# Performance work log

Measured on AMD Instinct MI355X. Metric: run time of the kernel, lower is better.

Reference implementation:

```python
import jax, jax.numpy as jnp
import numpy as np

HEAD_NUMS = 8
LN_EPS = 1e-5


def _layernorm(x, g, b):
    m = jnp.mean(x, axis=-1, keepdims=True)
    v = jnp.var(x, axis=-1, keepdims=True)
    return (x - m) * jax.lax.rsqrt(v + LN_EPS) * g + b


def setup_inputs() -> dict:
    key = jax.random.key(0)
    ks = jax.random.split(key, 6)
    B, S, D = 4, 2048, 512
    x = jax.random.normal(ks[0], (B, S, D), dtype=jnp.float32)
    W1 = jax.random.normal(ks[1], (4 * D, D), dtype=jnp.float32) * 0.02
    b1 = jnp.zeros((4 * D,), dtype=jnp.float32)
    ln_g = jnp.ones((D,), dtype=jnp.float32)
    ln_b = jnp.zeros((D,), dtype=jnp.float32)
    W2 = jax.random.normal(ks[2], (D, D), dtype=jnp.float32) * 0.02
    b2 = jnp.zeros((D,), dtype=jnp.float32)
    return {"x": x, "W1": W1, "b1": b1, "ln_g": ln_g, "ln_b": ln_b, "W2": W2, "b2": b2}


def reference(x, W1, b1, ln_g, ln_b, W2, b2):
    B, S, D = x.shape
    H = HEAD_NUMS
    hd = D // H
    # fused qkv+gate projection with SiLU (HSTU style)
    h = jax.nn.silu(x @ W1.T + b1)                   # [B,S,4D]
    h = h.reshape(B, S, 4, H, hd)                    # split into gate,q,k,v
    gate = jnp.transpose(h[:, :, 0], (0, 2, 1, 3))   # [B,H,S,hd]
    q = jnp.transpose(h[:, :, 1], (0, 2, 1, 3))
    k = jnp.transpose(h[:, :, 2], (0, 2, 1, 3))
    v = jnp.transpose(h[:, :, 3], (0, 2, 1, 3))
    scale = 1.0 / np.sqrt(hd).astype(np.float32)
    scores = jnp.einsum('bhsd,bhtd->bhst', q, k) * scale   # [B,H,S,S]
    causal = jnp.tril(jnp.ones((S, S), dtype=bool))        # allowed: t <= s
    # silu replaces softmax; masked (future) positions contribute 0
    # (mathematical limit of silu(-inf) is 0)
    a = jnp.where(causal, jax.nn.silu(scores), 0.0)
    o = jnp.einsum('bhst,bhtd->bhsd', a, v)                # [B,H,S,hd]
    o = jnp.transpose(o, (0, 2, 1, 3)).reshape(B, S, D)
    normed = _layernorm(o, ln_g, ln_b)
    gate_f = jnp.transpose(gate, (0, 2, 1, 3)).reshape(B, S, D)
    return (normed * gate_f) @ W2.T + b2
```

## Files before the change

kernel.cpp:

```cpp
#include <hip/hip_runtime.h>
#include <hip/hip_bf16.h>
#include <cstdint>


typedef __attribute__((ext_vector_type(8))) short short8;
typedef __attribute__((ext_vector_type(4))) float f32x4;

__device__ __forceinline__ unsigned short f2bf(float f) {
  union { float f; unsigned u; } v; v.f = f;
  unsigned r = v.u + 0x7FFFu + ((v.u >> 16) & 1u);
  return (unsigned short)(r >> 16);
}
__device__ __forceinline__ float bf2f(unsigned short h) {
  union { unsigned u; float f; } v; v.u = ((unsigned)h) << 16; return v.f;
}
__device__ __forceinline__ float fast_rcp(float x) {
#if __has_builtin(__builtin_amdgcn_rcpf)
  return __builtin_amdgcn_rcpf(x);
#else
  return 1.0f / x;
#endif
}
__device__ __forceinline__ float fast_exp2(float x) {
#if __has_builtin(__builtin_amdgcn_exp2f)
  return __builtin_amdgcn_exp2f(x);
#else
  return exp2f(x);
#endif
}
__device__ __forceinline__ float silu_f(float x) {
  return x * fast_rcp(1.0f + fast_exp2(-1.442695041f * x));
}
__device__ __forceinline__ unsigned pk2(float lo, float hi) {
  union { __hip_bfloat162 b; unsigned u; } cv;
  cv.b = __float22bfloat162_rn(make_float2(lo, hi));
  return cv.u;
}
__device__ __forceinline__ void gl_lds16(const void* g, void* l) {
  __builtin_amdgcn_global_load_lds(
      (const __attribute__((address_space(1))) void*)g,
      (__attribute__((address_space(3))) void*)l, 16, 0, 0);
}

__global__ void convert_kernel(const float* __restrict__ x, const float* __restrict__ w1,
                               const float* __restrict__ w2,
                               unsigned short* __restrict__ xb, unsigned short* __restrict__ w1b,
                               unsigned short* __restrict__ w2b) {
  int i = blockIdx.x * 256 + threadIdx.x;
  const float* s; unsigned short* d;
  if (i < 1048576) { s = x; d = xb; }
  else if (i < 1048576 + 262144) { i -= 1048576; s = w1; d = w1b; }
  else { i -= (1048576 + 262144); if (i >= 65536) return; s = w2; d = w2b; }
  float4 f = ((const float4*)s)[i];
  uint2 o; o.x = pk2(f.x, f.y); o.y = pk2(f.z, f.w);
  ((uint2*)d)[i] = o;
}

__global__ __launch_bounds__(256, 2) void gemm1_kernel(
    const unsigned short* __restrict__ xb,
    const unsigned short* __restrict__ w1b,
    const float* __restrict__ b1,
    unsigned short* __restrict__ h,
    unsigned short* __restrict__ vt)
{
  __shared__ __align__(16) unsigned short smem[16896];
  unsigned short* As = smem;
  unsigned short* Bs = smem + 8192;
  const int tid = threadIdx.x;
  const int w = tid >> 6, l = tid & 63;
  const int bm = blockIdx.x & 63, bn = blockIdx.x >> 6;
  const int wm = w & 1, wn = w >> 1;
  const int quad = l >> 4, lc = l & 15, lc7 = lc & 7;
  const int r8 = l >> 3, c8 = (l & 7) ^ r8;

  f32x4 acc[4][4] = {};
  const unsigned short* ga = xb + (size_t)(bm * 128 + w * 32 + r8) * 512 + c8 * 8;
  const unsigned short* gb = w1b + (size_t)(bn * 128 + w * 32 + r8) * 512 + c8 * 8;

  for (int kt = 0; kt < 512; kt += 64) {
#pragma unroll
    for (int i = 0; i < 4; ++i) {
      gl_lds16(ga + i * 8 * 512 + kt, As + (w * 4 + i) * 512);
      gl_lds16(gb + i * 8 * 512 + kt, Bs + (w * 4 + i) * 512);
    }
    __syncthreads();
#pragma unroll
    for (int kk = 0; kk < 2; ++kk) {
      short8 af[4], bf[4];
#pragma unroll
      for (int mt = 0; mt < 4; ++mt)
        af[mt] = *(const short8*)(As + (wm * 64 + mt * 16 + lc) * 64 +
                                  (((kk * 4 + quad) ^ lc7) * 8));
#pragma unroll
      for (int nt = 0; nt < 4; ++nt)
        bf[nt] = *(const short8*)(Bs + (wn * 64 + nt * 16 + lc) * 64 +
                                  (((kk * 4 + quad) ^ lc7) * 8));
#pragma unroll
      for (int mt = 0; mt < 4; ++mt)
#pragma unroll
        for (int nt = 0; nt < 4; ++nt)
          acc[mt][nt] = __builtin_amdgcn_mfma_f32_16x16x32_bf16(af[mt], bf[nt], acc[mt][nt], 0, 0, 0);
    }
    __syncthreads();
  }

  unsigned short* T = smem;
  const int sec = bn >> 2;
  if (sec == 3) {
#pragma unroll
    for (int nt = 0; nt < 4; ++nt) {
      const int nl = wn * 64 + nt * 16 + lc;
      const float bias = b1[bn * 128 + nl];
#pragma unroll
      for (int mt = 0; mt < 4; ++mt) {
        const int sl = wm * 64 + mt * 16 + quad * 4;
        uint2 pk;
        pk.x = pk2(silu_f(acc[mt][nt][0] + bias), silu_f(acc[mt][nt][1] + bias));
        pk.y = pk2(silu_f(acc[mt][nt][2] + bias), silu_f(acc[mt][nt][3] + bias));
        *(uint2*)(T + nl * 132 + sl) = pk;
      }
    }
  } else {
    const float osc = (sec == 1) ? 0.125f : 1.0f;
#pragma unroll
    for (int nt = 0; nt < 4; ++nt) {
      const int nl = wn * 64 + nt * 16 + lc;
      const float bias = b1[bn * 128 + nl];
#pragma unroll
      for (int mt = 0; mt < 4; ++mt) {
        const int sl = wm * 64 + mt * 16 + quad * 4;
#pragma unroll
        for (int r = 0; r < 4; ++r)
          T[(sl + r) * 132 + nl] = f2bf(silu_f(acc[mt][nt][r] + bias) * osc);
      }
    }
  }
  __syncthreads();
  const int rrow = tid >> 4, rcol = (tid & 15) * 8;
  if (sec == 3) {
    const int bq = bm >> 4, sbase = (bm & 15) * 128;
#pragma unroll
    for (int p = 0; p < 8; ++p) {
      const int row = p * 16 + rrow;
      const int n = bn * 128 + row, hh = (n >> 6) & 7, d = n & 63;
      *(short8*)(vt + (size_t)((bq * 8 + hh) * 64 + d) * 2048 + sbase + rcol) =
          *(const short8*)(T + row * 132 + rcol);
    }
  } else {
#pragma unroll
    for (int p = 0; p < 8; ++p) {
      const int row = p * 16 + rrow;
      *(short8*)(h + (size_t)(bm * 128 + row) * 2048 + bn * 128 + rcol) =
          *(const short8*)(T + row * 132 + rcol);
    }
  }
}

__global__ __launch_bounds__(256, 3) void attn_kernel(
    const unsigned short* __restrict__ h,
    const unsigned short* __restrict__ vt,
    float* __restrict__ o)
{
  __shared__ __align__(16) unsigned short Ks[128 * 64];
  __shared__ __align__(16) unsigned short Vs[64 * 128];
  __shared__ __align__(16) unsigned short Ps[64 * 136];
  const int tid = threadIdx.x;
  const int w = tid >> 6, l = tid & 63;
  const int bh = blockIdx.x & 31;
  const int qi = 31 - (blockIdx.x >> 5);
  const int b = bh >> 3, hh = bh & 7;
  const int quad = l >> 4, lc = l & 15, lc7 = lc & 7;
  const int r8 = l >> 3, c8 = (l & 7) ^ r8;
  const int wm = w & 1, wn = w >> 1;
  const int q0 = qi * 64;
  const int nk = (qi >> 1) + 1;

  {
    const unsigned short* qg =
        h + (size_t)(b * 2048 + q0 + w * 16 + r8) * 2048 + 512 + hh * 64 + c8 * 8;
#pragma unroll
    for (int i = 0; i < 2; ++i)
      gl_lds16(qg + (size_t)i * 8 * 2048, Ks + (w * 2 + i) * 512);
  }
  __syncthreads();
  short8 qf[2][2];
#pragma unroll
  for (int nt = 0; nt < 2; ++nt)
#pragma unroll
    for (int kk = 0; kk < 2; ++kk)
      qf[nt][kk] = *(const short8*)(Ks + (wn * 32 + nt * 16 + lc) * 64 +
                                    (((kk * 4 + quad) ^ lc7) * 8));

  f32x4 oacc[4] = {};

  const unsigned short* kg =
      h + (size_t)(b * 2048 + w * 32 + r8) * 2048 + 1024 + hh * 64 + c8 * 8;
  const int vrow = l >> 4, vcol = l & 15;
  const unsigned short* vgE =
      vt + (size_t)(bh * 64 + w * 16 + vrow) * 2048 + ((vcol ^ vrow) * 8);
  const unsigned short* vgO =
      vt + (size_t)(bh * 64 + w * 16 + vrow) * 2048 + ((vcol ^ vrow ^ 4) * 8);

  for (int ti = 0; ti < nk; ++ti) {
    __syncthreads();
    const int toff = ti * 128;
#pragma unroll
    for (int i = 0; i < 4; ++i) {
      gl_lds16(kg + (size_t)(toff + i * 8) * 2048, Ks + (w * 4 + i) * 512);
      const unsigned short* vsrc = ((i & 1) ? vgO : vgE) + (size_t)(i * 4) * 2048 + toff;
      gl_lds16(vsrc, Vs + (w * 4 + i) * 512);
    }
    __syncthreads();

    f32x4 sc[4][2] = {};
#pragma unroll
    for (int kk = 0; kk < 2; ++kk) {
      short8 kf[4];
#pragma unroll
      for (int mt = 0; mt < 4; ++mt)
        kf[mt] = *(const short8*)(Ks + (wm * 64 + mt * 16 + lc) * 64 +
                                  (((kk * 4 + quad) ^ lc7) * 8));
#pragma unroll
      for (int mt = 0; mt < 4; ++mt)
#pragma unroll
        for (int nt = 0; nt < 2; ++nt)
          sc[mt][nt] = __builtin_amdgcn_mfma_f32_16x16x32_bf16(kf[mt], qf[nt][kk], sc[mt][nt], 0, 0, 0);
    }

    if (ti < nk - 1) {
#pragma unroll
      for (int mt = 0; mt < 4; ++mt) {
        const int tloc = wm * 64 + mt * 16 + quad * 4;
#pragma unroll
        for (int nt = 0; nt < 2; ++nt) {
          const int qloc = wn * 32 + nt * 16 + lc;
          uint2 pk;
          pk.x = pk2(silu_f(sc[mt][nt][0]), silu_f(sc[mt][nt][1]));
          pk.y = pk2(silu_f(sc[mt][nt][2]), silu_f(sc[mt][nt][3]));
          *(uint2*)(Ps + qloc * 136 + tloc) = pk;
        }
      }
    } else {
#pragma unroll
      for (int mt = 0; mt < 4; ++mt) {
        const int tloc = wm * 64 + mt * 16 + quad * 4;
        const int tg = toff + tloc;
#pragma unroll
        for (int nt = 0; nt < 2; ++nt) {
          const int qloc = wn * 32 + nt * 16 + lc;
          const int qg = q0 + qloc;
          float v0 = (tg + 0 <= qg) ? silu_f(sc[mt][nt][0]) : 0.0f;
          float v1 = (tg + 1 <= qg) ? silu_f(sc[mt][nt][1]) : 0.0f;
          float v2 = (tg + 2 <= qg) ? silu_f(sc[mt][nt][2]) : 0.0f;
          float v3 = (tg + 3 <= qg) ? silu_f(sc[mt][nt][3]) : 0.0f;
          uint2 pk; pk.x = pk2(v0, v1); pk.y = pk2(v2, v3);
          *(uint2*)(Ps + qloc * 136 + tloc) = pk;
        }
      }
    }
    __syncthreads();

#pragma unroll
    for (int ks = 0; ks < 4; ++ks) {
      short8 pf = *(const short8*)(Ps + (w * 16 + lc) * 136 + ks * 32 + quad * 8);
#pragma unroll
      for (int nt = 0; nt < 4; ++nt) {
        short8 vf = *(const short8*)(Vs + (nt * 16 + lc) * 128 +
                                     (((ks * 4 + quad) ^ lc7) * 8));
        oacc[nt] = __builtin_amdgcn_mfma_f32_16x16x32_bf16(pf, vf, oacc[nt], 0, 0, 0);
      }
    }
  }

  float* og = o + (size_t)(b * 2048 + q0 + w * 16) * 512 + hh * 64;
#pragma unroll
  for (int nt = 0; nt < 4; ++nt)
#pragma unroll
    for (int r = 0; r < 4; ++r)
      og[(quad * 4 + r) * 512 + nt * 16 + lc] = oacc[nt][r];
}

__global__ __launch_bounds__(256) void ln_gate_kernel(
    const float* __restrict__ o, const unsigned short* __restrict__ h,
    const float* __restrict__ lng, const float* __restrict__ lnb,
    unsigned short* __restrict__ y) {
  const int row = blockIdx.x * 4 + (threadIdx.x >> 6);
  const int l = threadIdx.x & 63;
  const float4* orow = (const float4*)(o + (size_t)row * 512);
  float4 a = orow[l * 2], c = orow[l * 2 + 1];
  float s0 = a.x + a.y + a.z + a.w + c.x + c.y + c.z + c.w;
#pragma unroll
  for (int off = 32; off > 0; off >>= 1) s0 += __shfl_xor(s0, off);
  const float mean = s0 * (1.0f / 512.0f);
  float dx[8] = {a.x - mean, a.y - mean, a.z - mean, a.w - mean,
                 c.x - mean, c.y - mean, c.z - mean, c.w - mean};
  float sq = 0.f;
#pragma unroll
  for (int j = 0; j < 8; ++j) sq += dx[j] * dx[j];
#pragma unroll
  for (int off = 32; off > 0; off >>= 1) sq += __shfl_xor(sq, off);
  const float inv = rsqrtf(sq * (1.0f / 512.0f) + 1e-5f);
  const float4* g4 = (const float4*)lng;
  const float4* b4 = (const float4*)lnb;
  float4 g0 = g4[l * 2], g1 = g4[l * 2 + 1], bb0 = b4[l * 2], bb1 = b4[l * 2 + 1];
  const unsigned short* grow = h + (size_t)row * 2048;
  ushort4 gr0 = *(const ushort4*)(grow + l * 8);
  ushort4 gr1 = *(const ushort4*)(grow + l * 8 + 4);
  float gg[8] = {g0.x, g0.y, g0.z, g0.w, g1.x, g1.y, g1.z, g1.w};
  float bbv[8] = {bb0.x, bb0.y, bb0.z, bb0.w, bb1.x, bb1.y, bb1.z, bb1.w};
  float gv[8] = {bf2f(gr0.x), bf2f(gr0.y), bf2f(gr0.z), bf2f(gr0.w),
                 bf2f(gr1.x), bf2f(gr1.y), bf2f(gr1.z), bf2f(gr1.w)};
  float r[8];
#pragma unroll
  for (int j = 0; j < 8; ++j) r[j] = (dx[j] * inv * gg[j] + bbv[j]) * gv[j];
  uint2 p0, p1;
  p0.x = pk2(r[0], r[1]); p0.y = pk2(r[2], r[3]);
  p1.x = pk2(r[4], r[5]); p1.y = pk2(r[6], r[7]);
  uint2* yrow = (uint2*)(y + (size_t)row * 512);
  yrow[l * 2] = p0;
  yrow[l * 2 + 1] = p1;
}

__global__ __launch_bounds__(256, 2) void gemm2_kernel(
    const unsigned short* __restrict__ yb,
    const unsigned short* __restrict__ w2b,
    const float* __restrict__ b2, float* __restrict__ out) {
  __shared__ __align__(16) unsigned short As[128 * 64];
  __shared__ __align__(16) unsigned short Bs[128 * 64];
  const int tid = threadIdx.x;
  const int w = tid >> 6, l = tid & 63;
  const int bm = blockIdx.x & 63, bn = blockIdx.x >> 6;
  const int wm = w & 1, wn = w >> 1;
  const int quad = l >> 4, lc = l & 15, lc7 = lc & 7;
  const int r8 = l >> 3, c8 = (l & 7) ^ r8;

  f32x4 acc[4][4] = {};
  const unsigned short* ga = yb + (size_t)(bm * 128 + w * 32 + r8) * 512 + c8 * 8;
  const unsigned short* gb = w2b + (size_t)(bn * 128 + w * 32 + r8) * 512 + c8 * 8;

  for (int kt = 0; kt < 512; kt += 64) {
#pragma unroll
    for (int i = 0; i < 4; ++i) {
      gl_lds16(ga + i * 8 * 512 + kt, As + (w * 4 + i) * 512);
      gl_lds16(gb + i * 8 * 512 + kt, Bs + (w * 4 + i) * 512);
    }
    __syncthreads();
#pragma unroll
    for (int kk = 0; kk < 2; ++kk) {
      short8 af[4], bf[4];
#pragma unroll
      for (int mt = 0; mt < 4; ++mt)
        af[mt] = *(const short8*)(As + (wm * 64 + mt * 16 + lc) * 64 +
                                  (((kk * 4 + quad) ^ lc7) * 8));
#pragma unroll
      for (int nt = 0; nt < 4; ++nt)
        bf[nt] = *(const short8*)(Bs + (wn * 64 + nt * 16 + lc) * 64 +
                                  (((kk * 4 + quad) ^ lc7) * 8));
#pragma unroll
      for (int mt = 0; mt < 4; ++mt)
#pragma unroll
        for (int nt = 0; nt < 4; ++nt)
          acc[mt][nt] = __builtin_amdgcn_mfma_f32_16x16x32_bf16(af[mt], bf[nt], acc[mt][nt], 0, 0, 0);
    }
    __syncthreads();
  }

#pragma unroll
  for (int nt = 0; nt < 4; ++nt) {
    const int n = bn * 128 + wn * 64 + nt * 16 + lc;
    const float bias = b2[n];
#pragma unroll
    for (int mt = 0; mt < 4; ++mt) {
      const int m0 = bm * 128 + wm * 64 + mt * 16 + quad * 4;
#pragma unroll
      for (int r = 0; r < 4; ++r)
        out[(size_t)(m0 + r) * 512 + n] = acc[mt][nt][r] + bias;
    }
  }
}

extern "C" void kernel_launch(void* const* d_in, const int* in_sizes, int n_in,
                              void* d_out, int out_size, void* d_ws, size_t ws_size,
                              hipStream_t stream) {
  const float* x = (const float*)d_in[0];
  const float* W1 = (const float*)d_in[1];
  const float* b1 = (const float*)d_in[2];
  const float* lng = (const float*)d_in[3];
  const float* lnb = (const float*)d_in[4];
  const float* W2 = (const float*)d_in[5];
  const float* b2 = (const float*)d_in[6];
  float* out = (float*)d_out;
  char* ws = (char*)d_ws;

  unsigned short* xb  = (unsigned short*)(ws);
  unsigned short* w1b = (unsigned short*)(ws + 8388608);
  unsigned short* w2b = (unsigned short*)(ws + 10485760);
  unsigned short* h   = (unsigned short*)(ws + 11010048);
  unsigned short* vt  = (unsigned short*)(ws + 44564480);
  float* o            = (float*)(ws + 52953088);
  unsigned short* yb  = (unsigned short*)(ws + 69730304);

  convert_kernel<<<5376, 256, 0, stream>>>(x, W1, W2, xb, w1b, w2b);
  gemm1_kernel<<<1024, 256, 0, stream>>>(xb, w1b, b1, h, vt);
  attn_kernel<<<1024, 256, 0, stream>>>(h, vt, o);
  ln_gate_kernel<<<2048, 256, 0, stream>>>(o, h, lng, lnb, yb);
  gemm2_kernel<<<256, 256, 0, stream>>>(yb, w2b, b2, out);
}
```

Measured before the change: 158.9 us.

## Keep attention P in registers via bpermute, split-K PV, smaller gemm2 tiles

The attention kernel no longer writes silu(scores) to a shared-memory P tile and syncs. It reshuffles the packed P fragments across lanes with ds_bpermute and feeds them straight into the PV MFMAs. Each wave pair now splits the key dimension, and partial outputs are reduced through shared memory at the end, which adds a cross-wave reduction step. Separately, gemm2 moves to 64x64 tiles with four times as many blocks to fill the GPU better, and the launch bounds of gemm1 and gemm2 rise to 3 waves per SIMD, which may add register pressure.

```diff
diff --git a/kernel.cpp b/kernel.cpp
--- a/kernel.cpp
+++ b/kernel.cpp
@@ -56,7 +56,7 @@
   ((uint2*)d)[i] = o;
 }
 
-__global__ __launch_bounds__(256, 2) void gemm1_kernel(
+__global__ __launch_bounds__(256, 3) void gemm1_kernel(
     const unsigned short* __restrict__ xb,
     const unsigned short* __restrict__ w1b,
     const float* __restrict__ b1,
@@ -161,9 +161,9 @@
     const unsigned short* __restrict__ vt,
     float* __restrict__ o)
 {
-  __shared__ __align__(16) unsigned short Ks[128 * 64];
-  __shared__ __align__(16) unsigned short Vs[64 * 128];
-  __shared__ __align__(16) unsigned short Ps[64 * 136];
+  __shared__ __align__(16) unsigned short smem[17408];
+  unsigned short* Ks = smem;
+  unsigned short* Vs = smem + 8192;
   const int tid = threadIdx.x;
   const int w = tid >> 6, l = tid & 63;
   const int bh = blockIdx.x & 31;
@@ -174,6 +174,9 @@
   const int wm = w & 1, wn = w >> 1;
   const int q0 = qi * 64;
   const int nk = (qi >> 1) + 1;
+  const int addrA = (((quad & 1) * 2) * 16 + lc) * 4;
+  const int addrB = addrA + 64;
+  const bool hiq = (quad >> 1) != 0;
 
   {
     const unsigned short* qg =
@@ -191,7 +194,7 @@
       qf[nt][kk] = *(const short8*)(Ks + (wn * 32 + nt * 16 + lc) * 64 +
                                     (((kk * 4 + quad) ^ lc7) * 8));
 
-  f32x4 oacc[4] = {};
+  f32x4 oacc[2][4] = {};
 
   const unsigned short* kg =
       h + (size_t)(b * 2048 + w * 32 + r8) * 2048 + 1024 + hh * 64 + c8 * 8;
@@ -227,57 +230,86 @@
           sc[mt][nt] = __builtin_amdgcn_mfma_f32_16x16x32_bf16(kf[mt], qf[nt][kk], sc[mt][nt], 0, 0, 0);
     }
 
+    unsigned pd[4][2][2];
     if (ti < nk - 1) {
 #pragma unroll
+      for (int mt = 0; mt < 4; ++mt)
+#pragma unroll
+        for (int nt = 0; nt < 2; ++nt) {
+          pd[mt][nt][0] = pk2(silu_f(sc[mt][nt][0]), silu_f(sc[mt][nt][1]));
+          pd[mt][nt][1] = pk2(silu_f(sc[mt][nt][2]), silu_f(sc[mt][nt][3]));
+        }
+    } else {
+#pragma unroll
       for (int mt = 0; mt < 4; ++mt) {
-        const int tloc = wm * 64 + mt * 16 + quad * 4;
+        const int tg = toff + wm * 64 + mt * 16 + quad * 4;
 #pragma unroll
         for (int nt = 0; nt < 2; ++nt) {
-          const int qloc = wn * 32 + nt * 16 + lc;
-          uint2 pk;
-          pk.x = pk2(silu_f(sc[mt][nt][0]), silu_f(sc[mt][nt][1]));
-          pk.y = pk2(silu_f(sc[mt][nt][2]), silu_f(sc[mt][nt][3]));
-          *(uint2*)(Ps + qloc * 136 + tloc) = pk;
-        }
-      }
-    } else {
-#pragma unroll
-      for (int mt = 0; mt < 4; ++mt) {
-        const int tloc = wm * 64 + mt * 16 + quad * 4;
-        const int tg = toff + tloc;
-#pragma unroll
-        for (int nt = 0; nt < 2; ++nt) {
-          const int qloc = wn * 32 + nt * 16 + lc;
-          const int qg = q0 + qloc;
+          const int qg = q0 + wn * 32 + nt * 16 + lc;
           float v0 = (tg + 0 <= qg) ? silu_f(sc[mt][nt][0]) : 0.0f;
           float v1 = (tg + 1 <= qg) ? silu_f(sc[mt][nt][1]) : 0.0f;
           float v2 = (tg + 2 <= qg) ? silu_f(sc[mt][nt][2]) : 0.0f;
           float v3 = (tg + 3 <= qg) ? silu_f(sc[mt][nt][3]) : 0.0f;
-          uint2 pk; pk.x = pk2(v0, v1); pk.y = pk2(v2, v3);
-          *(uint2*)(Ps + qloc * 136 + tloc) = pk;
+          pd[mt][nt][0] = pk2(v0, v1);
+          pd[mt][nt][1] = pk2(v2, v3);
         }
       }
     }
-    __syncthreads();
-
-#pragma unroll
-    for (int ks = 0; ks < 4; ++ks) {
-      short8 pf = *(const short8*)(Ps + (w * 16 + lc) * 136 + ks * 32 + quad * 8);
-#pragma unroll
-      for (int nt = 0; nt < 4; ++nt) {
-        short8 vf = *(const short8*)(Vs + (nt * 16 + lc) * 128 +
-                                     (((ks * 4 + quad) ^ lc7) * 8));
-        oacc[nt] = __builtin_amdgcn_mfma_f32_16x16x32_bf16(pf, vf, oacc[nt], 0, 0, 0);
+
+#pragma unroll
+    for (int c = 0; c < 2; ++c) {
+      short8 vf[4];
+#pragma unroll
+      for (int dt = 0; dt < 4; ++dt)
+        vf[dt] = *(const short8*)(Vs + (dt * 16 + lc) * 128 +
+                                  (((wm * 8 + c * 4 + quad) ^ lc7) * 8));
+#pragma unroll
+      for (int nt = 0; nt < 2; ++nt) {
+        int lo0 = __builtin_amdgcn_ds_bpermute(addrA, (int)pd[2 * c][nt][0]);
+        int hi0 = __builtin_amdgcn_ds_bpermute(addrA, (int)pd[2 * c + 1][nt][0]);
+        int lo1 = __builtin_amdgcn_ds_bpermute(addrA, (int)pd[2 * c][nt][1]);
+        int hi1 = __builtin_amdgcn_ds_bpermute(addrA, (int)pd[2 * c + 1][nt][1]);
+        int lo2 = __builtin_amdgcn_ds_bpermute(addrB, (int)pd[2 * c][nt][0]);
+        int hi2 = __builtin_amdgcn_ds_bpermute(addrB, (int)pd[2 * c + 1][nt][0]);
+        int lo3 = __builtin_amdgcn_ds_bpermute(addrB, (int)pd[2 * c][nt][1]);
+        int hi3 = __builtin_amdgcn_ds_bpermute(addrB, (int)pd[2 * c + 1][nt][1]);
+        int4 pfu;
+        pfu.x = hiq ? hi0 : lo0;
+        pfu.y = hiq ? hi1 : lo1;
+        pfu.z = hiq ? hi2 : lo2;
+        pfu.w = hiq ? hi3 : lo3;
+        short8 pf = *(short8*)&pfu;
+#pragma unroll
+        for (int dt = 0; dt < 4; ++dt)
+          oacc[nt][dt] = __builtin_amdgcn_mfma_f32_16x16x32_bf16(pf, vf[dt], oacc[nt][dt], 0, 0, 0);
       }
     }
   }
 
-  float* og = o + (size_t)(b * 2048 + q0 + w * 16) * 512 + hh * 64;
-#pragma unroll
-  for (int nt = 0; nt < 4; ++nt)
-#pragma unroll
-    for (int r = 0; r < 4; ++r)
-      og[(quad * 4 + r) * 512 + nt * 16 + lc] = oacc[nt][r];
+  __syncthreads();
+  float* R = (float*)smem;
+  if (wm == 1) {
+#pragma unroll
+    for (int nt = 0; nt < 2; ++nt)
+#pragma unroll
+      for (int dt = 0; dt < 4; ++dt)
+        *(f32x4*)(R + (dt * 16 + lc) * 68 + wn * 32 + nt * 16 + quad * 4) = oacc[nt][dt];
+  }
+  __syncthreads();
+  if (wm == 0) {
+    float* og = o + (size_t)(b * 2048 + q0 + wn * 32) * 512 + hh * 64;
+#pragma unroll
+    for (int nt = 0; nt < 2; ++nt)
+#pragma unroll
+      for (int dt = 0; dt < 4; ++dt) {
+        f32x4 rr = *(const f32x4*)(R + (dt * 16 + lc) * 68 + wn * 32 + nt * 16 + quad * 4);
+        f32x4 v = oacc[nt][dt];
+        v[0] += rr[0]; v[1] += rr[1]; v[2] += rr[2]; v[3] += rr[3];
+#pragma unroll
+        for (int r = 0; r < 4; ++r)
+          og[(nt * 16 + quad * 4 + r) * 512 + dt * 16 + lc] = v[r];
+      }
+  }
 }
 
 __global__ __launch_bounds__(256) void ln_gate_kernel(
@@ -321,57 +353,57 @@
   yrow[l * 2 + 1] = p1;
 }
 
-__global__ __launch_bounds__(256, 2) void gemm2_kernel(
+__global__ __launch_bounds__(256, 3) void gemm2_kernel(
     const unsigned short* __restrict__ yb,
     const unsigned short* __restrict__ w2b,
     const float* __restrict__ b2, float* __restrict__ out) {
-  __shared__ __align__(16) unsigned short As[128 * 64];
-  __shared__ __align__(16) unsigned short Bs[128 * 64];
+  __shared__ __align__(16) unsigned short As[64 * 64];
+  __shared__ __align__(16) unsigned short Bs[64 * 64];
   const int tid = threadIdx.x;
   const int w = tid >> 6, l = tid & 63;
-  const int bm = blockIdx.x & 63, bn = blockIdx.x >> 6;
+  const int bm = blockIdx.x & 127, bn = blockIdx.x >> 7;
   const int wm = w & 1, wn = w >> 1;
   const int quad = l >> 4, lc = l & 15, lc7 = lc & 7;
   const int r8 = l >> 3, c8 = (l & 7) ^ r8;
 
-  f32x4 acc[4][4] = {};
-  const unsigned short* ga = yb + (size_t)(bm * 128 + w * 32 + r8) * 512 + c8 * 8;
-  const unsigned short* gb = w2b + (size_t)(bn * 128 + w * 32 + r8) * 512 + c8 * 8;
+  f32x4 acc[2][2] = {};
+  const unsigned short* ga = yb + (size_t)(bm * 64 + w * 16 + r8) * 512 + c8 * 8;
+  const unsigned short* gb = w2b + (size_t)(bn * 64 + w * 16 + r8) * 512 + c8 * 8;
 
   for (int kt = 0; kt < 512; kt += 64) {
 #pragma unroll
-    for (int i = 0; i < 4; ++i) {
-      gl_lds16(ga + i * 8 * 512 + kt, As + (w * 4 + i) * 512);
-      gl_lds16(gb + i * 8 * 512 + kt, Bs + (w * 4 + i) * 512);
+    for (int j = 0; j < 2; ++j) {
+      gl_lds16(ga + j * 8 * 512 + kt, As + (w * 2 + j) * 512);
+      gl_lds16(gb + j * 8 * 512 + kt, Bs + (w * 2 + j) * 512);
     }
     __syncthreads();
 #pragma unroll
     for (int kk = 0; kk < 2; ++kk) {
-      short8 af[4], bf[4];
-#pragma unroll
-      for (int mt = 0; mt < 4; ++mt)
-        af[mt] = *(const short8*)(As + (wm * 64 + mt * 16 + lc) * 64 +
+      short8 af[2], bf[2];
+#pragma unroll
+      for (int mt = 0; mt < 2; ++mt)
+        af[mt] = *(const short8*)(As + (wm * 32 + mt * 16 + lc) * 64 +
                                   (((kk * 4 + quad) ^ lc7) * 8));
 #pragma unroll
-      for (int nt = 0; nt < 4; ++nt)
-        bf[nt] = *(const short8*)(Bs + (wn * 64 + nt * 16 + lc) * 64 +
+      for (int nt = 0; nt < 2; ++nt)
+        bf[nt] = *(const short8*)(Bs + (wn * 32 + nt * 16 + lc) * 64 +
                                   (((kk * 4 + quad) ^ lc7) * 8));
 #pragma unroll
-      for (int mt = 0; mt < 4; ++mt)
-#pragma unroll
-        for (int nt = 0; nt < 4; ++nt)
+      for (int mt = 0; mt < 2; ++mt)
+#pragma unroll
+        for (int nt = 0; nt < 2; ++nt)
           acc[mt][nt] = __builtin_amdgcn_mfma_f32_16x16x32_bf16(af[mt], bf[nt], acc[mt][nt], 0, 0, 0);
     }
     __syncthreads();
   }
 
 #pragma unroll
-  for (int nt = 0; nt < 4; ++nt) {
-    const int n = bn * 128 + wn * 64 + nt * 16 + lc;
+  for (int nt = 0; nt < 2; ++nt) {
+    const int n = bn * 64 + wn * 32 + nt * 16 + lc;
     const float bias = b2[n];
 #pragma unroll
-    for (int mt = 0; mt < 4; ++mt) {
-      const int m0 = bm * 128 + wm * 64 + mt * 16 + quad * 4;
+    for (int mt = 0; mt < 2; ++mt) {
+      const int m0 = bm * 64 + wm * 32 + mt * 16 + quad * 4;
 #pragma unroll
       for (int r = 0; r < 4; ++r)
         out[(size_t)(m0 + r) * 512 + n] = acc[mt][nt][r] + bias;
@@ -404,5 +436,5 @@
   gemm1_kernel<<<1024, 256, 0, stream>>>(xb, w1b, b1, h, vt);
   attn_kernel<<<1024, 256, 0, stream>>>(h, vt, o);
   ln_gate_kernel<<<2048, 256, 0, stream>>>(o, h, lng, lnb, yb);
-  gemm2_kernel<<<256, 256, 0, stream>>>(yb, w2b, b2, out);
-}
+  gemm2_kernel<<<1024, 256, 0, stream>>>(yb, w2b, b2, out);
+}
```

Measured after the change: 165.3 us. 4.0% more time.
